# Kernel optimization log

Hardware: AMD Instinct MI355X
Metric: run time of the kernel (lower is better)

The kernel has to match this reference:

```python
import jax, jax.numpy as jnp
import numpy as np

N_NODES = 50000
N_EDGES = 800000
IN_DIM = 256
OUT_DIM = 768
D_SCALE = OUT_DIM // 3  # 256, must equal IN_DIM so repeated conv application type-checks
SCALES = [1, 2, 4]


def setup_inputs() -> dict:
    key = jax.random.key(0)
    ks = jax.random.split(key, 12)
    x = jax.random.normal(ks[0], (N_NODES, IN_DIM), dtype=jnp.float32)
    edge_index = jax.random.randint(ks[1], (2, N_EDGES), 0, N_NODES, dtype=jnp.int64)
    edge_attr = jax.random.uniform(ks[2], (N_EDGES, 1), dtype=jnp.float32)
    s = 1.0 / np.sqrt(IN_DIM)
    W1 = jax.random.uniform(ks[3], (IN_DIM, D_SCALE), jnp.float32, -s, s)
    b1 = jnp.zeros((D_SCALE,), jnp.float32)
    W2 = jax.random.uniform(ks[4], (IN_DIM, D_SCALE), jnp.float32, -s, s)
    b2 = jnp.zeros((D_SCALE,), jnp.float32)
    W3 = jax.random.uniform(ks[5], (IN_DIM, D_SCALE), jnp.float32, -s, s)
    b3 = jnp.zeros((D_SCALE,), jnp.float32)
    sp = 1.0 / np.sqrt(OUT_DIM)
    Wp = jax.random.uniform(ks[6], (OUT_DIM, OUT_DIM), jnp.float32, -sp, sp)
    bp = jax.random.uniform(ks[7], (OUT_DIM,), jnp.float32, -sp, sp)
    gamma = jnp.ones((OUT_DIM,), jnp.float32)
    beta = jnp.zeros((OUT_DIM,), jnp.float32)
    return {"x": x, "edge_index": edge_index, "edge_attr": edge_attr,
            "W1": W1, "b1": b1, "W2": W2, "b2": b2, "W3": W3, "b3": b3,
            "Wp": Wp, "bp": bp, "gamma": gamma, "beta": beta}


def _gcn_conv(x, src, dst, norm, W, b):
    # PyG GCNConv: h = x @ W; out[i] = sum_{(j->i)} norm_e * h[j]; + bias
    h = x @ W                                   # [N, D]
    msg = h[src] * norm[:, None]                # [E+N, D] edge gather (memory-bound)
    out = jax.ops.segment_sum(msg, dst, num_segments=N_NODES)
    return out + b


def reference(x, edge_index, edge_attr, W1, b1, W2, b2, W3, b3, Wp, bp, gamma, beta):
    ew = edge_attr.squeeze(-1)
    src = edge_index[0]
    dst = edge_index[1]
    # add self-loops with weight 1 (GCNConv default, fill_value=1)
    loop = jnp.arange(N_NODES, dtype=src.dtype)
    src_a = jnp.concatenate([src, loop])
    dst_a = jnp.concatenate([dst, loop])
    w_a = jnp.concatenate([ew, jnp.ones((N_NODES,), ew.dtype)])
    deg = jax.ops.segment_sum(w_a, dst_a, num_segments=N_NODES)
    dinv = jnp.where(deg > 0, jax.lax.rsqrt(deg), 0.0)
    norm = dinv[src_a] * w_a * dinv[dst_a]      # symmetric normalization per edge

    feats = []
    for (W, b), scale in zip([(W1, b1), (W2, b2), (W3, b3)], SCALES):
        f = x
        for _ in range(scale):
            f = _gcn_conv(f, src_a, dst_a, norm, W, b)
        feats.append(f)
    out = jnp.concatenate(feats, axis=1)        # [N, OUT_DIM]
    out = out @ Wp + bp
    mu = jnp.mean(out, axis=-1, keepdims=True)
    var = jnp.var(out, axis=-1, keepdims=True)
    out = (out - mu) * jax.lax.rsqrt(var + 1e-5) * gamma + beta
    return jax.nn.gelu(out, approximate=False)
```

## Files before the change

### kernel.cpp

```cpp
#include <hip/hip_runtime.h>
#include <math.h>

#define NN 50000
#define NE 800000
#define DIN 256
#define DOUT 768
#define NPAD 50176

typedef _Float16 half8 __attribute__((ext_vector_type(8)));
typedef _Float16 half4 __attribute__((ext_vector_type(4)));
typedef float    f32x4 __attribute__((ext_vector_type(4)));

__global__ void init_deg_cnt(float* __restrict__ deg, int* __restrict__ cnt) {
    int i = blockIdx.x * 256 + threadIdx.x;
    if (i < NN) { deg[i] = 1.0f; cnt[i] = 0; }
}

__global__ void edge_deg_cnt(const int* __restrict__ ei, const float* __restrict__ ea,
                             float* __restrict__ deg, int* __restrict__ cnt) {
    int e = blockIdx.x * 256 + threadIdx.x;
    if (e >= NE) return;
    int dst = ei[NE + e];
    atomicAdd(&deg[dst], ea[e]);
    atomicAdd(&cnt[dst], 1);
}

__global__ void compute_dinv(const float* __restrict__ deg, float* __restrict__ dinv) {
    int i = blockIdx.x * 256 + threadIdx.x;
    if (i < NN) { float d = deg[i]; dinv[i] = d > 0.f ? rsqrtf(d) : 0.f; }
}

__global__ __launch_bounds__(1024) void scan_kernel(
        const int* __restrict__ cnt, int* __restrict__ row_ptr,
        int* __restrict__ cursor) {
    __shared__ int ssum[1024];
    int t = threadIdx.x;
    const int chunk = (NN + 1023) / 1024;
    int beg = t * chunk;
    int end = beg + chunk; if (end > NN) end = NN;
    int s = 0;
    for (int i = beg; i < end; ++i) s += cnt[i];
    ssum[t] = s;
    __syncthreads();
    if (t == 0) {
        int run = 0;
        for (int i = 0; i < 1024; ++i) { int v = ssum[i]; ssum[i] = run; run += v; }
    }
    __syncthreads();
    int run = ssum[t];
    for (int i = beg; i < end; ++i) {
        row_ptr[i] = run; cursor[i] = run; run += cnt[i];
    }
    if (t == 0) row_ptr[NN] = NE;
}

__global__ void edge_scatter(const int* __restrict__ ei, const float* __restrict__ ea,
                             const float* __restrict__ dinv, int* __restrict__ cursor,
                             int* __restrict__ col, float* __restrict__ val) {
    int e = blockIdx.x * 256 + threadIdx.x;
    if (e >= NE) return;
    int s = ei[e];
    int d = ei[NE + e];
    int pos = atomicAdd(&cursor[d], 1);
    col[pos] = s;
    val[pos] = dinv[s] * ea[e] * dinv[d];
}

__global__ void x2h_kernel(const float* __restrict__ x, _Float16* __restrict__ Xh) {
    int i = blockIdx.x * 256 + threadIdx.x;
    if (i >= NN * DIN / 4) return;
    float4 v = ((const float4*)x)[i];
    half4 h; h[0] = (_Float16)v.x; h[1] = (_Float16)v.y;
    h[2] = (_Float16)v.z; h[3] = (_Float16)v.w;
    ((half4*)Xh)[i] = h;
}

__global__ __launch_bounds__(256) void agg_kernel(
        const _Float16* __restrict__ Gin, int sIn,
        _Float16* __restrict__ Gout, int sOut,
        const float* __restrict__ Rin, float* __restrict__ Rout,
        const int* __restrict__ rowp, const int* __restrict__ colv,
        const float* __restrict__ val, const float* __restrict__ dinv) {
    int node = blockIdx.x * 4 + (threadIdx.x >> 6);
    if (node >= NN) return;
    int lane = threadIdx.x & 63;
    int sub = lane >> 5, l32 = lane & 31;
    const _Float16* gb = Gin + l32 * 8;
    float acc[8] = {0.f, 0.f, 0.f, 0.f, 0.f, 0.f, 0.f, 0.f};
    float racc = 0.f;
    int beg = rowp[node], end = rowp[node + 1];
    int k = beg;
    for (; k + 4 <= end; k += 4) {
        int e0 = k + sub, e1 = k + 2 + sub;
        int   c0 = colv[e0], c1 = colv[e1];
        float v0 = val[e0],  v1 = val[e1];
        half8 g0 = *(const half8*)(gb + (size_t)c0 * sIn);
        half8 g1 = *(const half8*)(gb + (size_t)c1 * sIn);
#pragma unroll
        for (int j = 0; j < 8; ++j)
            acc[j] += v0 * (float)g0[j] + v1 * (float)g1[j];
        if (l32 == 0)
            racc += v0 * (Rin ? Rin[c0] : 1.f) + v1 * (Rin ? Rin[c1] : 1.f);
    }
    for (; k < end; k += 2) {
        int e = k + sub;
        if (e < end) {
            int c = colv[e]; float v = val[e];
            half8 g = *(const half8*)(gb + (size_t)c * sIn);
#pragma unroll
            for (int j = 0; j < 8; ++j) acc[j] += v * (float)g[j];
            if (l32 == 0) racc += v * (Rin ? Rin[c] : 1.f);
        }
    }
#pragma unroll
    for (int j = 0; j < 8; ++j) acc[j] += __shfl_xor(acc[j], 32);
    racc += __shfl_xor(racc, 32);
    float dv = dinv[node], sv = dv * dv;
    half8 gs = *(const half8*)(gb + (size_t)node * sIn);
#pragma unroll
    for (int j = 0; j < 8; ++j) acc[j] += sv * (float)gs[j];
    if (sub == 0) {
        half8 o;
#pragma unroll
        for (int j = 0; j < 8; ++j) o[j] = (_Float16)acc[j];
        *(half8*)(Gout + (size_t)node * sOut + l32 * 8) = o;
    }
    if (Rout && lane == 0)
        Rout[node] = racc + sv * (Rin ? Rin[node] : 1.f);
}

__global__ __launch_bounds__(256) void wp1(
        const float* __restrict__ W2, const float* __restrict__ W3,
        const float* __restrict__ b2, const float* __restrict__ b3,
        float* __restrict__ W2sq, float* __restrict__ W3_2,
        float* __restrict__ bw2, float* __restrict__ bw3a) {
    int b = blockIdx.x, j = threadIdx.x;
    const float* A; const float* B; float* C;
    if (b < 256)      { A = W2 + b * 256;         B = W2; C = W2sq + b * 256; }
    else if (b < 512) { A = W3 + (b - 256) * 256; B = W3; C = W3_2 + (b - 256) * 256; }
    else if (b == 512){ A = b2;                   B = W2; C = bw2; }
    else              { A = b3;                   B = W3; C = bw3a; }
    float s = 0.f;
#pragma unroll 8
    for (int k = 0; k < 256; ++k) s += A[k] * B[k * 256 + j];
    C[j] = s;
}

__global__ __launch_bounds__(256) void wp2(
        const float* __restrict__ W3_2, const float* __restrict__ W3,
        const float* __restrict__ bw3a,
        float* __restrict__ W3_4, float* __restrict__ bw3b) {
    int b = blockIdx.x, j = threadIdx.x;
    const float* A; const float* B; float* C;
    if (b < 256) { A = W3_2 + b * 256; B = W3_2; C = W3_4 + b * 256; }
    else         { A = bw3a;           B = W3;   C = bw3b; }
    float s = 0.f;
#pragma unroll 8
    for (int k = 0; k < 256; ++k) s += A[k] * B[k * 256 + j];
    C[j] = s;
}

__global__ __launch_bounds__(256) void wp3(
        const float* __restrict__ W1, const float* __restrict__ W2sq,
        const float* __restrict__ W3_4, const float* __restrict__ Wp,
        const float* __restrict__ W3, const float* __restrict__ bw3b,
        _Float16* __restrict__ Mt, float* __restrict__ bw3c) {
    int b = blockIdx.x, j = threadIdx.x;
    if (b == 768) {
        float s = 0.f;
#pragma unroll 8
        for (int k = 0; k < 256; ++k) s += bw3b[k] * W3[k * 256 + j];
        bw3c[j] = s;
        return;
    }
    int kk = b;
    int blk = kk >> 8;
    const float* A = (blk == 0) ? (W1 + kk * 256)
                   : (blk == 1) ? (W2sq + (kk - 256) * 256)
                                : (W3_4 + (kk - 512) * 256);
    const float* B = Wp + (size_t)(blk * 256) * 768;
    float s0 = 0.f, s1 = 0.f, s2 = 0.f;
#pragma unroll 4
    for (int m = 0; m < 256; ++m) {
        float a = A[m];
        const float* br = B + (size_t)m * 768;
        s0 += a * br[j]; s1 += a * br[j + 256]; s2 += a * br[j + 512];
    }
    Mt[(size_t)j * 768 + kk]         = (_Float16)s0;
    Mt[(size_t)(j + 256) * 768 + kk] = (_Float16)s1;
    Mt[(size_t)(j + 512) * 768 + kk] = (_Float16)s2;
}

__global__ __launch_bounds__(256) void wp4(
        const float* __restrict__ Wp,
        const float* __restrict__ b1, const float* __restrict__ b2,
        const float* __restrict__ b3, const float* __restrict__ bp,
        const float* __restrict__ bw2, const float* __restrict__ bw3a,
        const float* __restrict__ bw3b, const float* __restrict__ bw3c,
        float* __restrict__ u1, float* __restrict__ u2,
        float* __restrict__ u3, float* __restrict__ c0) {
    int vec = blockIdx.x / 3, chunk = blockIdx.x % 3;
    int j = chunk * 256 + threadIdx.x;
    const float* P1 = Wp;
    const float* P2 = Wp + (size_t)256 * 768;
    const float* P3 = Wp + (size_t)512 * 768;
    float s = 0.f;
    if (vec == 0) {
#pragma unroll 8
        for (int k = 0; k < 256; ++k) s += bw2[k] * P2[(size_t)k * 768 + j];
#pragma unroll 8
        for (int k = 0; k < 256; ++k) s += bw3a[k] * P3[(size_t)k * 768 + j];
        u1[j] = s;
    } else if (vec == 1) {
#pragma unroll 8
        for (int k = 0; k < 256; ++k) s += bw3b[k] * P3[(size_t)k * 768 + j];
        u2[j] = s;
    } else if (vec == 2) {
#pragma unroll 8
        for (int k = 0; k < 256; ++k) s += bw3c[k] * P3[(size_t)k * 768 + j];
        u3[j] = s;
    } else {
#pragma unroll 8
        for (int k = 0; k < 256; ++k) s += b1[k] * P1[(size_t)k * 768 + j];
#pragma unroll 8
        for (int k = 0; k < 256; ++k) s += b2[k] * P2[(size_t)k * 768 + j];
#pragma unroll 8
        for (int k = 0; k < 256; ++k) s += b3[k] * P3[(size_t)k * 768 + j];
        c0[j] = s + bp[j];
    }
}

__device__ inline void g2lds16(const void* g, void* l) {
    __builtin_amdgcn_global_load_lds(
        (__attribute__((address_space(1))) void*)g,
        (__attribute__((address_space(3))) void*)l, 16, 0, 0);
}

__global__ __launch_bounds__(256) void gemm_mfma(
        const _Float16* __restrict__ A,
        const _Float16* __restrict__ Bt,
        float* __restrict__ C, int M,
        const float* __restrict__ R1, const float* __restrict__ R2,
        const float* __restrict__ R3,
        const float* __restrict__ u1, const float* __restrict__ u2,
        const float* __restrict__ u3, const float* __restrict__ c0) {
    __shared__ _Float16 As[128 * 32];
    __shared__ _Float16 Bs[128 * 32];
    const int tid  = threadIdx.x;
    const int wid  = tid >> 6;
    const int lane = tid & 63;
    const int bm = blockIdx.y * 128;
    const int bn = blockIdx.x * 128;
    const int wm = (wid >> 1) * 64;
    const int wn = (wid & 1) * 64;
    const int l15  = lane & 15;
    const int quad = lane >> 4;

    f32x4 acc[4][4] = {};

    const int srow_in_grp = lane >> 2;
    const int schunk      = lane & 3;

    for (int k0 = 0; k0 < DOUT; k0 += 32) {
#pragma unroll
        for (int q = 0; q < 2; ++q) {
            int row = wid * 32 + q * 16 + srow_in_grp;
            int gchunk = (schunk - ((row >> 1) & 3)) & 3;
            const _Float16* ga = A  + (size_t)(bm + row) * DOUT + k0 + gchunk * 8;
            const _Float16* gb = Bt + (size_t)(bn + row) * DOUT + k0 + gchunk * 8;
            g2lds16(ga, As + (size_t)(wid * 32 + q * 16) * 32);
            g2lds16(gb, Bs + (size_t)(wid * 32 + q * 16) * 32);
        }
        __syncthreads();
        half8 af[4], bfr[4];
#pragma unroll
        for (int i = 0; i < 4; ++i) {
            int ra = wm + i * 16 + l15;
            int pa = (quad + ((ra >> 1) & 3)) & 3;
            af[i] = *(const half8*)(As + (size_t)ra * 32 + pa * 8);
            int rb = wn + i * 16 + l15;
            int pb = (quad + ((rb >> 1) & 3)) & 3;
            bfr[i] = *(const half8*)(Bs + (size_t)rb * 32 + pb * 8);
        }
#pragma unroll
        for (int mi = 0; mi < 4; ++mi)
#pragma unroll
            for (int ni = 0; ni < 4; ++ni)
                acc[mi][ni] = __builtin_amdgcn_mfma_f32_16x16x32_f16(
                    af[mi], bfr[ni], acc[mi][ni], 0, 0, 0);
        __syncthreads();
    }

    float e0[4], e1[4], e2[4], e3[4];
#pragma unroll
    for (int ni = 0; ni < 4; ++ni) {
        int gc = bn + wn + ni * 16 + l15;
        e0[ni] = c0[gc]; e1[ni] = u1[gc]; e2[ni] = u2[gc]; e3[ni] = u3[gc];
    }
#pragma unroll
    for (int mi = 0; mi < 4; ++mi) {
#pragma unroll
        for (int r = 0; r < 4; ++r) {
            int gr = bm + wm + mi * 16 + quad * 4 + r;
            if (gr >= M) continue;
            float r1 = R1[gr], r2 = R2[gr], r3 = R3[gr];
#pragma unroll
            for (int ni = 0; ni < 4; ++ni) {
                int gc = bn + wn + ni * 16 + l15;
                C[(size_t)gr * DOUT + gc] =
                    acc[mi][ni][r] + e0[ni] + r1 * e1[ni] + r2 * e2[ni] + r3 * e3[ni];
            }
        }
    }
}

__global__ __launch_bounds__(256) void ln_gelu_kernel(float* __restrict__ out,
        const float* __restrict__ gamma, const float* __restrict__ beta) {
    int row = blockIdx.x;
    int t = threadIdx.x;
    float* p = out + (size_t)row * DOUT;
    float x0 = p[t], x1 = p[t + 256], x2 = p[t + 512];
    float s = x0 + x1 + x2;
    float s2 = x0 * x0 + x1 * x1 + x2 * x2;
    __shared__ float red[8];
    int wave = t >> 6, lane = t & 63;
#pragma unroll
    for (int m = 1; m < 64; m <<= 1) {
        s += __shfl_xor(s, m);
        s2 += __shfl_xor(s2, m);
    }
    if (lane == 0) { red[wave] = s; red[4 + wave] = s2; }
    __syncthreads();
    float S = red[0] + red[1] + red[2] + red[3];
    float S2 = red[4] + red[5] + red[6] + red[7];
    float mu = S * (1.f / 768.f);
    float var = S2 * (1.f / 768.f) - mu * mu;
    float inv = rsqrtf(var + 1e-5f);
    const float kk = 0.70710678118654752f;
#pragma unroll
    for (int i = 0; i < 3; ++i) {
        int c = t + 256 * i;
        float x = (i == 0) ? x0 : (i == 1) ? x1 : x2;
        float y = (x - mu) * inv * gamma[c] + beta[c];
        p[c] = 0.5f * y * (1.f + erff(y * kk));
    }
}

extern "C" void kernel_launch(void* const* d_in, const int* in_sizes, int n_in,
                              void* d_out, int out_size, void* d_ws, size_t ws_size,
                              hipStream_t stream) {
    const float* x     = (const float*)d_in[0];
    const int*   ei    = (const int*)d_in[1];
    const float* ea    = (const float*)d_in[2];
    const float* W1    = (const float*)d_in[3];
    const float* b1    = (const float*)d_in[4];
    const float* W2    = (const float*)d_in[5];
    const float* b2    = (const float*)d_in[6];
    const float* W3    = (const float*)d_in[7];
    const float* b3    = (const float*)d_in[8];
    const float* Wp    = (const float*)d_in[9];
    const float* bp    = (const float*)d_in[10];
    const float* gamma = (const float*)d_in[11];
    const float* beta  = (const float*)d_in[12];
    float* out = (float*)d_out;

    char* w = (char*)d_ws;
    auto alloc = [&](size_t bytes) -> void* {
        void* p = (void*)w;
        w += (bytes + 255) & ~(size_t)255;
        return p;
    };
    _Float16* Acat = (_Float16*)alloc((size_t)NPAD * DOUT * 2);
    _Float16* Xh   = (_Float16*)alloc((size_t)NN * DIN * 2);
    _Float16* G3h  = (_Float16*)alloc((size_t)NN * DIN * 2);
    _Float16* Mt   = (_Float16*)alloc((size_t)DOUT * DOUT * 2);
    int*   col    = (int*)alloc((size_t)NE * 4);
    float* val    = (float*)alloc((size_t)NE * 4);
    float* deg    = (float*)alloc((size_t)NN * 4);
    float* dinv   = (float*)alloc((size_t)NN * 4);
    int*   cnt    = (int*)alloc((size_t)NN * 4);
    int*   rowp   = (int*)alloc((size_t)(NN + 1) * 4);
    int*   cursor = (int*)alloc((size_t)NN * 4);
    float* R1     = (float*)alloc((size_t)NN * 4);
    float* R2     = (float*)alloc((size_t)NN * 4);
    float* R3     = (float*)alloc((size_t)NN * 4);
    float* W2sq   = (float*)alloc(256 * 256 * 4);
    float* W3_2   = (float*)alloc(256 * 256 * 4);
    float* W3_4   = (float*)alloc(256 * 256 * 4);
    float* bw2    = (float*)alloc(256 * 4);
    float* bw3a   = (float*)alloc(256 * 4);
    float* bw3b   = (float*)alloc(256 * 4);
    float* bw3c   = (float*)alloc(256 * 4);
    float* u1     = (float*)alloc(768 * 4);
    float* u2     = (float*)alloc(768 * 4);
    float* u3     = (float*)alloc(768 * 4);
    float* c0     = (float*)alloc(768 * 4);

    const int nb_n = (NN + 255) / 256;
    const int nb_e = (NE + 255) / 256;

    init_deg_cnt<<<nb_n, 256, 0, stream>>>(deg, cnt);
    edge_deg_cnt<<<nb_e, 256, 0, stream>>>(ei, ea, deg, cnt);
    compute_dinv<<<nb_n, 256, 0, stream>>>(deg, dinv);
    scan_kernel<<<1, 1024, 0, stream>>>(cnt, rowp, cursor);
    edge_scatter<<<nb_e, 256, 0, stream>>>(ei, ea, dinv, cursor, col, val);

    x2h_kernel<<<(NN * DIN / 4 + 255) / 256, 256, 0, stream>>>(x, Xh);

    wp1<<<514, 256, 0, stream>>>(W2, W3, b2, b3, W2sq, W3_2, bw2, bw3a);
    wp2<<<257, 256, 0, stream>>>(W3_2, W3, bw3a, W3_4, bw3b);
    wp3<<<769, 256, 0, stream>>>(W1, W2sq, W3_4, Wp, W3, bw3b, Mt, bw3c);
    wp4<<<12, 256, 0, stream>>>(Wp, b1, b2, b3, bp, bw2, bw3a, bw3b, bw3c,
                                u1, u2, u3, c0);

    const int nb_a = (NN + 3) / 4;
    agg_kernel<<<nb_a, 256, 0, stream>>>(Xh, DIN,          Acat + 0,   DOUT, nullptr, R1, rowp, col, val, dinv);
    agg_kernel<<<nb_a, 256, 0, stream>>>(Acat + 0,   DOUT, Acat + 256, DOUT, R1,      R2, rowp, col, val, dinv);
    agg_kernel<<<nb_a, 256, 0, stream>>>(Acat + 256, DOUT, G3h,        DIN,  R2,      R3, rowp, col, val, dinv);
    agg_kernel<<<nb_a, 256, 0, stream>>>(G3h,        DIN,  Acat + 512, DOUT, nullptr, nullptr, rowp, col, val, dinv);

    dim3 grid(DOUT / 128, (NN + 127) / 128);
    gemm_mfma<<<grid, 256, 0, stream>>>(Acat, Mt, out, NN, R1, R2, R3, u1, u2, u3, c0);

    ln_gelu_kernel<<<NN, 256, 0, stream>>>(out, gamma, beta);
}
```

Measured before the change: 969.3 us.

## Widen aggregation per-lane loads, double-buffer GEMM LDS, and swizzle GEMM block order

The aggregation kernel now has each lane of a wave own 4 features of a node and walk the edges serially, unrolled by 8, instead of splitting the edges between half-waves and reducing with shuffles. This raises the number of independent gathers in flight and removes the cross-half reduction. The GEMM double-buffers its LDS tiles so the next K-slice loads while MFMAs run on the current one. It also remaps block IDs into an XCD-style interleaved order over a padded grid. These changes double LDS use per block, and the grid now launches blocks over padded rows, which relies on Acat being allocated to NPAD rows.

```diff
diff --git a/kernel.cpp b/kernel.cpp
--- a/kernel.cpp
+++ b/kernel.cpp
@@ -75,6 +75,10 @@
     ((half4*)Xh)[i] = h;
 }
 
+__device__ inline float rv(const float* __restrict__ R, int c) {
+    return R ? R[c] : 1.f;
+}
+
 __global__ __launch_bounds__(256) void agg_kernel(
         const _Float16* __restrict__ Gin, int sIn,
         _Float16* __restrict__ Gout, int sOut,
@@ -84,47 +88,66 @@
     int node = blockIdx.x * 4 + (threadIdx.x >> 6);
     if (node >= NN) return;
     int lane = threadIdx.x & 63;
-    int sub = lane >> 5, l32 = lane & 31;
-    const _Float16* gb = Gin + l32 * 8;
-    float acc[8] = {0.f, 0.f, 0.f, 0.f, 0.f, 0.f, 0.f, 0.f};
+    const _Float16* gb = Gin + lane * 4;
+    float acc[4] = {0.f, 0.f, 0.f, 0.f};
     float racc = 0.f;
     int beg = rowp[node], end = rowp[node + 1];
     int k = beg;
+    for (; k + 8 <= end; k += 8) {
+        int   c0 = colv[k+0], c1 = colv[k+1], c2 = colv[k+2], c3 = colv[k+3];
+        int   c4 = colv[k+4], c5 = colv[k+5], c6 = colv[k+6], c7 = colv[k+7];
+        float v0 = val[k+0], v1 = val[k+1], v2 = val[k+2], v3 = val[k+3];
+        float v4 = val[k+4], v5 = val[k+5], v6 = val[k+6], v7 = val[k+7];
+        half4 g0 = *(const half4*)(gb + (size_t)c0 * sIn);
+        half4 g1 = *(const half4*)(gb + (size_t)c1 * sIn);
+        half4 g2 = *(const half4*)(gb + (size_t)c2 * sIn);
+        half4 g3 = *(const half4*)(gb + (size_t)c3 * sIn);
+        half4 g4 = *(const half4*)(gb + (size_t)c4 * sIn);
+        half4 g5 = *(const half4*)(gb + (size_t)c5 * sIn);
+        half4 g6 = *(const half4*)(gb + (size_t)c6 * sIn);
+        half4 g7 = *(const half4*)(gb + (size_t)c7 * sIn);
+#pragma unroll
+        for (int j = 0; j < 4; ++j)
+            acc[j] += v0 * (float)g0[j] + v1 * (float)g1[j]
+                    + v2 * (float)g2[j] + v3 * (float)g3[j]
+                    + v4 * (float)g4[j] + v5 * (float)g5[j]
+                    + v6 * (float)g6[j] + v7 * (float)g7[j];
+        if (Rout)
+            racc += v0 * rv(Rin, c0) + v1 * rv(Rin, c1)
+                  + v2 * rv(Rin, c2) + v3 * rv(Rin, c3)
+                  + v4 * rv(Rin, c4) + v5 * rv(Rin, c5)
+                  + v6 * rv(Rin, c6) + v7 * rv(Rin, c7);
+    }
     for (; k + 4 <= end; k += 4) {
-        int e0 = k + sub, e1 = k + 2 + sub;
-        int   c0 = colv[e0], c1 = colv[e1];
-        float v0 = val[e0],  v1 = val[e1];
-        half8 g0 = *(const half8*)(gb + (size_t)c0 * sIn);
-        half8 g1 = *(const half8*)(gb + (size_t)c1 * sIn);
-#pragma unroll
-        for (int j = 0; j < 8; ++j)
-            acc[j] += v0 * (float)g0[j] + v1 * (float)g1[j];
-        if (l32 == 0)
-            racc += v0 * (Rin ? Rin[c0] : 1.f) + v1 * (Rin ? Rin[c1] : 1.f);
-    }
-    for (; k < end; k += 2) {
-        int e = k + sub;
-        if (e < end) {
-            int c = colv[e]; float v = val[e];
-            half8 g = *(const half8*)(gb + (size_t)c * sIn);
-#pragma unroll
-            for (int j = 0; j < 8; ++j) acc[j] += v * (float)g[j];
-            if (l32 == 0) racc += v * (Rin ? Rin[c] : 1.f);
-        }
-    }
-#pragma unroll
-    for (int j = 0; j < 8; ++j) acc[j] += __shfl_xor(acc[j], 32);
-    racc += __shfl_xor(racc, 32);
+        int   c0 = colv[k+0], c1 = colv[k+1], c2 = colv[k+2], c3 = colv[k+3];
+        float v0 = val[k+0], v1 = val[k+1], v2 = val[k+2], v3 = val[k+3];
+        half4 g0 = *(const half4*)(gb + (size_t)c0 * sIn);
+        half4 g1 = *(const half4*)(gb + (size_t)c1 * sIn);
+        half4 g2 = *(const half4*)(gb + (size_t)c2 * sIn);
+        half4 g3 = *(const half4*)(gb + (size_t)c3 * sIn);
+#pragma unroll
+        for (int j = 0; j < 4; ++j)
+            acc[j] += v0 * (float)g0[j] + v1 * (float)g1[j]
+                    + v2 * (float)g2[j] + v3 * (float)g3[j];
+        if (Rout)
+            racc += v0 * rv(Rin, c0) + v1 * rv(Rin, c1)
+                  + v2 * rv(Rin, c2) + v3 * rv(Rin, c3);
+    }
+    for (; k < end; ++k) {
+        int c = colv[k]; float v = val[k];
+        half4 g = *(const half4*)(gb + (size_t)c * sIn);
+#pragma unroll
+        for (int j = 0; j < 4; ++j) acc[j] += v * (float)g[j];
+        if (Rout) racc += v * rv(Rin, c);
+    }
     float dv = dinv[node], sv = dv * dv;
-    half8 gs = *(const half8*)(gb + (size_t)node * sIn);
-#pragma unroll
-    for (int j = 0; j < 8; ++j) acc[j] += sv * (float)gs[j];
-    if (sub == 0) {
-        half8 o;
-#pragma unroll
-        for (int j = 0; j < 8; ++j) o[j] = (_Float16)acc[j];
-        *(half8*)(Gout + (size_t)node * sOut + l32 * 8) = o;
-    }
+    half4 gs = *(const half4*)(gb + (size_t)node * sIn);
+#pragma unroll
+    for (int j = 0; j < 4; ++j) acc[j] += sv * (float)gs[j];
+    half4 o;
+#pragma unroll
+    for (int j = 0; j < 4; ++j) o[j] = (_Float16)acc[j];
+    *(half4*)(Gout + (size_t)node * sOut + lane * 4) = o;
     if (Rout && lane == 0)
         Rout[node] = racc + sv * (Rin ? Rin[node] : 1.f);
 }
@@ -244,13 +267,15 @@
         const float* __restrict__ R3,
         const float* __restrict__ u1, const float* __restrict__ u2,
         const float* __restrict__ u3, const float* __restrict__ c0) {
-    __shared__ _Float16 As[128 * 32];
-    __shared__ _Float16 Bs[128 * 32];
+    __shared__ _Float16 As[2][128 * 32];
+    __shared__ _Float16 Bs[2][128 * 32];
     const int tid  = threadIdx.x;
     const int wid  = tid >> 6;
     const int lane = tid & 63;
-    const int bm = blockIdx.y * 128;
-    const int bn = blockIdx.x * 128;
+    const int lid  = blockIdx.y * (DOUT / 128) + blockIdx.x;
+    const int pair = (lid & 7) * (NPAD / 128 * (DOUT / 128) / 8) + (lid >> 3);
+    const int bm = (pair / (DOUT / 128)) * 128;
+    const int bn = (pair % (DOUT / 128)) * 128;
     const int wm = (wid >> 1) * 64;
     const int wn = (wid & 1) * 64;
     const int l15  = lane & 15;
@@ -261,26 +286,33 @@
     const int srow_in_grp = lane >> 2;
     const int schunk      = lane & 3;
 
-    for (int k0 = 0; k0 < DOUT; k0 += 32) {
+    auto stage = [&](int buf, int k0) {
 #pragma unroll
         for (int q = 0; q < 2; ++q) {
             int row = wid * 32 + q * 16 + srow_in_grp;
             int gchunk = (schunk - ((row >> 1) & 3)) & 3;
             const _Float16* ga = A  + (size_t)(bm + row) * DOUT + k0 + gchunk * 8;
             const _Float16* gb = Bt + (size_t)(bn + row) * DOUT + k0 + gchunk * 8;
-            g2lds16(ga, As + (size_t)(wid * 32 + q * 16) * 32);
-            g2lds16(gb, Bs + (size_t)(wid * 32 + q * 16) * 32);
+            g2lds16(ga, &As[buf][(size_t)(wid * 32 + q * 16) * 32]);
+            g2lds16(gb, &Bs[buf][(size_t)(wid * 32 + q * 16) * 32]);
         }
-        __syncthreads();
+    };
+
+    const int NT = DOUT / 32;
+    stage(0, 0);
+    __syncthreads();
+    int cur = 0;
+    for (int t = 0; t < NT; ++t) {
+        if (t + 1 < NT) stage(cur ^ 1, (t + 1) * 32);
         half8 af[4], bfr[4];
 #pragma unroll
         for (int i = 0; i < 4; ++i) {
             int ra = wm + i * 16 + l15;
             int pa = (quad + ((ra >> 1) & 3)) & 3;
-            af[i] = *(const half8*)(As + (size_t)ra * 32 + pa * 8);
+            af[i] = *(const half8*)(&As[cur][(size_t)ra * 32 + pa * 8]);
             int rb = wn + i * 16 + l15;
             int pb = (quad + ((rb >> 1) & 3)) & 3;
-            bfr[i] = *(const half8*)(Bs + (size_t)rb * 32 + pb * 8);
+            bfr[i] = *(const half8*)(&Bs[cur][(size_t)rb * 32 + pb * 8]);
         }
 #pragma unroll
         for (int mi = 0; mi < 4; ++mi)
@@ -289,6 +321,7 @@
                 acc[mi][ni] = __builtin_amdgcn_mfma_f32_16x16x32_f16(
                     af[mi], bfr[ni], acc[mi][ni], 0, 0, 0);
         __syncthreads();
+        cur ^= 1;
     }
 
     float e0[4], e1[4], e2[4], e3[4];
@@ -419,7 +452,7 @@
     agg_kernel<<<nb_a, 256, 0, stream>>>(Acat + 256, DOUT, G3h,        DIN,  R2,      R3, rowp, col, val, dinv);
     agg_kernel<<<nb_a, 256, 0, stream>>>(G3h,        DIN,  Acat + 512, DOUT, nullptr, nullptr, rowp, col, val, dinv);
 
-    dim3 grid(DOUT / 128, (NN + 127) / 128);
+    dim3 grid(DOUT / 128, NPAD / 128);
     gemm_mfma<<<grid, 256, 0, stream>>>(Acat, Mt, out, NN, R1, R2, R3, u1, u2, u3, c0);
 
     ln_gelu_kernel<<<NN, 256, 0, stream>>>(out, gamma, beta);
```

Result: no change. 973.6 us (+0.4%).
